# Kernel tuning notes

Hardware: AMD Instinct MI355X
Metric: run time of the kernel (lower is better)

## Reference

```python
import jax, jax.numpy as jnp
import numpy as np

B, S, D = 2, 2048, 1024
NUM_HEAD = 8
HEAD_SIZE = D // NUM_HEAD


def setup_inputs() -> dict:
    key = jax.random.key(0)
    ks = jax.random.split(key, 10)
    scale = 1.0 / np.sqrt(D)
    inp = {
        "q": jax.random.normal(ks[0], (B, S, D), dtype=jnp.float32),
        "k": jax.random.normal(ks[1], (B, S, D), dtype=jnp.float32),
        "v": jax.random.normal(ks[2], (B, S, D), dtype=jnp.float32),
        "mask": jax.random.bernoulli(ks[3], 0.1, (B, 1, S, S)),
        "Wq": jax.random.normal(ks[4], (D, D), dtype=jnp.float32) * scale,
        "bq": jnp.zeros((D,), dtype=jnp.float32),
        "Wk": jax.random.normal(ks[5], (D, D), dtype=jnp.float32) * scale,
        "bk": jnp.zeros((D,), dtype=jnp.float32),
        "Wv": jax.random.normal(ks[6], (D, D), dtype=jnp.float32) * scale,
        "bv": jnp.zeros((D,), dtype=jnp.float32),
    }
    return inp


def _split_heads(x):
    # [B,S,D] -> [B,H,S,Hd]
    b, s, _ = x.shape
    return x.reshape(b, s, NUM_HEAD, HEAD_SIZE).transpose(0, 2, 1, 3)


def reference(q, k, v, mask, Wq, bq, Wk, bk, Wv, bv):
    Q = _split_heads(q @ Wq + bq)
    K = _split_heads(k @ Wk + bk)
    V = _split_heads(v @ Wv + bv)
    # scores [B,H,S,S]; NB: mask applied BEFORE scaling, as in the original
    QK = jnp.einsum("bhqd,bhkd->bhqk", Q, K)
    QK = jnp.where(mask, jnp.float32(-1e6), QK)
    QK = QK / jnp.float32(np.sqrt(HEAD_SIZE))
    attn = jax.nn.softmax(QK, axis=-1)  # dropout is identity in eval mode
    ctx = jnp.einsum("bhqk,bhkd->bhqd", attn, V)
    out = ctx.transpose(0, 2, 1, 3).reshape(q.shape[0], q.shape[1], D)
    return out
```

## Files before the change

### kernel.cpp

```cpp
#include <hip/hip_runtime.h>

typedef __bf16 bf16;
typedef __attribute__((ext_vector_type(8))) __bf16 bf16x8;
typedef __attribute__((ext_vector_type(4))) __bf16 bf16x4;
typedef __attribute__((ext_vector_type(4))) float f32x4;
typedef __attribute__((ext_vector_type(4))) float fvec4;

#define NB 2
#define SEQ 2048
#define DM 1024
#define NH 8
#define HD 128

#define QSCL (0.08838834764831845f * 1.4426950408889634f)

#define AS1 __attribute__((address_space(1)))
#define AS3 __attribute__((address_space(3)))

__global__ __launch_bounds__(256) void prep_kernel(
    const float* __restrict__ qi, const float* __restrict__ ki,
    const float* __restrict__ vi,
    const float* __restrict__ Wq, const float* __restrict__ Wk,
    const float* __restrict__ Wv,
    const unsigned int* __restrict__ mask32,
    bf16* __restrict__ Xc, bf16* __restrict__ Wt,
    unsigned int* __restrict__ flag)
{
    const int z   = blockIdx.y;
    const int tid = threadIdx.x;
    __shared__ __align__(16) bf16 tile[64][80];
    __shared__ unsigned int sred[256];

    if (z < 3) {
        const float* src = (z == 0) ? qi : (z == 1) ? ki : vi;
        bf16* dst = Xc + (size_t)z * ((size_t)NB * SEQ * DM);
        const size_t base = (size_t)blockIdx.x * 4096 + (size_t)tid * 16;
        fvec4 f[4];
        #pragma unroll
        for (int j = 0; j < 4; j++)
            f[j] = *(const fvec4*)(src + base + j * 4);
        bf16x8 h0, h1;
        #pragma unroll
        for (int e = 0; e < 8; e++) {
            h0[e] = (bf16)f[e >> 2][e & 3];
            h1[e] = (bf16)f[2 + (e >> 2)][e & 3];
        }
        *(bf16x8*)(dst + base)     = h0;
        *(bf16x8*)(dst + base + 8) = h1;
    } else if (z < 6) {
        if (blockIdx.x >= 256) return;
        const float* W = (z == 3) ? Wq : (z == 4) ? Wk : Wv;
        bf16* dst = Wt + (size_t)(z - 3) * ((size_t)DM * DM);
        const float scl = (z == 3) ? QSCL : 1.0f;
        const int n0 = (blockIdx.x & 15) * 64;
        const int k0 = (blockIdx.x >> 4) * 64;
        #pragma unroll
        for (int p = 0; p < 4; p++) {
            const int r = p * 16 + (tid >> 4);
            const int c = (tid & 15) * 4;
            const fvec4 wv = *(const fvec4*)(W + (size_t)(k0 + r) * DM + n0 + c);
            #pragma unroll
            for (int j = 0; j < 4; j++)
                tile[c + j][r] = (bf16)(wv[j] * scl);
        }
        __syncthreads();
        #pragma unroll
        for (int p = 0; p < 2; p++) {
            const int row = p * 32 + (tid >> 3);
            const int ch  = tid & 7;
            const bf16x8 hv = *(const bf16x8*)(&tile[row][ch * 8]);
            *(bf16x8*)(dst + (size_t)(n0 + row) * DM + k0 + ch * 8) = hv;
        }
    } else {
        if (blockIdx.x != 0) return;
        unsigned int f = 0;
        for (int i = tid; i < 1024; i += 256) {
            const unsigned int w2 = mask32[i];
            if ((w2 & 0xFEFEFEFEu) == 0u && (w2 & 0xFFFFFF00u) != 0u) f = 1;
        }
        sred[tid] = f;
        __syncthreads();
        if (tid == 0) {
            unsigned int r = 0;
            for (int i = 0; i < 256; i++) r |= sred[i];
            *flag = r;
        }
    }
}

__global__ __launch_bounds__(256) void proj_kernel(
    const bf16* __restrict__ Xc, const bf16* __restrict__ Wt,
    const float* __restrict__ bq, const float* __restrict__ bk,
    const float* __restrict__ bv,
    bf16* __restrict__ Qo, bf16* __restrict__ Ko, bf16* __restrict__ Vto,
    const void* __restrict__ mask, const unsigned int* __restrict__ flag,
    unsigned long long* __restrict__ bits)
{
    __shared__ __align__(16) bf16 As[2][128 * 64];
    __shared__ __align__(16) bf16 Bs[2][128 * 64];

    const int pz = blockIdx.z;
    const int tid = threadIdx.x;

    if (pz == 3) {
        const bool bytem = (*flag & 1u) != 0;
        const int wid = blockIdx.y * 8 + blockIdx.x;
        const int t   = wid * 256 + tid;
        unsigned short* const bits16o = (unsigned short*)bits;
        #pragma unroll 2
        for (int it = 0; it < 8; ++it) {
            const size_t e0 = ((size_t)it * 65536 + t) * 16;
            unsigned int b16 = 0;
            if (bytem) {
                const uint4 wv = *(const uint4*)((const unsigned char*)mask + e0);
                const unsigned int wd[4] = {wv.x, wv.y, wv.z, wv.w};
                #pragma unroll
                for (int j = 0; j < 4; j++) {
                    b16 |= ((wd[j] & 0x000000FFu) ? 1u : 0u) << (4 * j + 0);
                    b16 |= ((wd[j] & 0x0000FF00u) ? 1u : 0u) << (4 * j + 1);
                    b16 |= ((wd[j] & 0x00FF0000u) ? 1u : 0u) << (4 * j + 2);
                    b16 |= ((wd[j] & 0xFF000000u) ? 1u : 0u) << (4 * j + 3);
                }
            } else {
                const unsigned int* mw = (const unsigned int*)mask + e0;
                #pragma unroll
                for (int j = 0; j < 4; j++) {
                    const uint4 wv = *(const uint4*)(mw + 4 * j);
                    b16 |= (wv.x ? 1u : 0u) << (4 * j + 0);
                    b16 |= (wv.y ? 1u : 0u) << (4 * j + 1);
                    b16 |= (wv.z ? 1u : 0u) << (4 * j + 2);
                    b16 |= (wv.w ? 1u : 0u) << (4 * j + 3);
                }
            }
            bits16o[e0 >> 4] = (unsigned short)b16;
        }
        return;
    }

    const bf16* X  = Xc + (size_t)pz * ((size_t)NB * SEQ * DM);
    const bf16* Bt = Wt + (size_t)pz * ((size_t)DM * DM);
    const float* bias = (pz == 0) ? bq : (pz == 1) ? bk : bv;
    const float bscl  = (pz == 0) ? QSCL : 1.0f;
    bf16* dst = (pz == 0) ? Qo : (pz == 1) ? Ko : Vto;

    const int lane = tid & 63;
    const int w    = tid >> 6;
    const int q16  = lane >> 4;
    const int l15  = lane & 15;

    const int lid  = (int)blockIdx.x + 8 * (int)blockIdx.y;
    const int nlid = (lid & 7) * 32 + (lid >> 3);
    const int m0 = (nlid >> 3) * 128;
    const int n0 = (nlid & 7) * 128;
    const int wm = (w >> 1) * 64;
    const int wn = (w & 1) * 64;

    auto stage = [&](int buf, int k0) {
        #pragma unroll
        for (int i = 0; i < 4; i++) {
            const int c   = i * 256 + tid;
            const int row = c >> 3;
            const int cir = c & 7;
            const bf16* src =
                X + (size_t)(m0 + row) * DM + k0 + ((cir ^ (row & 7)) << 3);
            __builtin_amdgcn_global_load_lds(
                (const AS1 void*)src,
                (AS3 void*)(&As[buf][c * 8]),
                16, 0, 0);
        }
        #pragma unroll
        for (int i = 0; i < 4; i++) {
            const int c   = i * 256 + tid;
            const int row = c >> 3;
            const int cir = c & 7;
            const bf16* src =
                Bt + (size_t)(n0 + row) * DM + k0 + ((cir ^ (row & 7)) << 3);
            __builtin_amdgcn_global_load_lds(
                (const AS1 void*)src,
                (AS3 void*)(&Bs[buf][c * 8]),
                16, 0, 0);
        }
    };

    f32x4 acc[4][4] = {};
    stage(0, 0);
    __syncthreads();
    int cur = 0;

    for (int kt = 0; kt < DM / 64; ++kt) {
        if (kt + 1 < DM / 64) stage(cur ^ 1, (kt + 1) * 64);
        const bf16* Asb = &As[cur][0];
        const bf16* Bsb = &Bs[cur][0];
        #pragma unroll
        for (int c2 = 0; c2 < 2; c2++) {
            bf16x8 af[4], bfr[4];
            #pragma unroll
            for (int mi = 0; mi < 4; mi++) {
                const int row = wm + mi * 16 + l15;
                af[mi] = *(const bf16x8*)(
                    Asb + row * 64 + (((c2 * 4 + q16) ^ (row & 7)) << 3));
            }
            #pragma unroll
            for (int ni = 0; ni < 4; ni++) {
                const int row = wn + ni * 16 + l15;
                bfr[ni] = *(const bf16x8*)(
                    Bsb + row * 64 + (((c2 * 4 + q16) ^ (row & 7)) << 3));
            }
            #pragma unroll
            for (int mi = 0; mi < 4; mi++)
                #pragma unroll
                for (int ni = 0; ni < 4; ni++)
                    acc[mi][ni] = __builtin_amdgcn_mfma_f32_16x16x32_bf16(
                        af[mi], bfr[ni], acc[mi][ni], 0, 0, 0);
        }
        __syncthreads();
        cur ^= 1;
    }

    float bias_v[4];
    #pragma unroll
    for (int ni = 0; ni < 4; ni++)
        bias_v[ni] = bias[n0 + wn + ni * 16 + l15];

    #pragma unroll
    for (int mi = 0; mi < 4; mi++) {
        #pragma unroll
        for (int ni = 0; ni < 4; ni++) {
            const int n  = n0 + wn + ni * 16 + l15;
            const int h  = n >> 7;
            const int hd = n & (HD - 1);
            #pragma unroll
            for (int r = 0; r < 4; r++) {
                const int m = m0 + wm + mi * 16 + q16 * 4 + r;
                const int b = m >> 11;
                const int s = m & (SEQ - 1);
                const float val = acc[mi][ni][r] + bias_v[ni] * bscl;
                size_t idx;
                if (pz == 2) {
                    const int s63 = s & 63;
                    const int nf  = s63 >> 4;
                    const int g   = (s63 >> 2) & 3;
                    const int rr  = s63 & 3;
                    const int slot = (nf >> 1) * 32 + g * 8 + (nf & 1) * 4 + rr;
                    const int sp = (s & ~63) | slot;
                    idx = ((size_t)(b * NH + h) * HD + hd) * SEQ + sp;
                } else {
                    idx = ((size_t)(b * NH + h) * SEQ + s) * HD + hd;
                }
                dst[idx] = (bf16)val;
            }
        }
    }
}

__global__ __launch_bounds__(256) void attn_kernel(
    const bf16* __restrict__ Q, const bf16* __restrict__ K,
    const bf16* __restrict__ Vt, const unsigned int* __restrict__ maskbits,
    float* __restrict__ out)
{
    __shared__ __align__(16) bf16 Ks[2][64 * 128];
    __shared__ __align__(16) bf16 Vs[2][128 * 64];

    const int tid  = threadIdx.x;
    const int lane = tid & 63;
    const int w    = tid >> 6;
    const int q16  = lane >> 4;
    const int l15  = lane & 15;
    const int l3   = l15 & 7;

    const int lid  = (int)blockIdx.x
                   + 32 * ((int)blockIdx.y + 8 * (int)blockIdx.z);
    const int nlid = (lid & 7) * 64 + (lid >> 3);
    const int q0  = (nlid & 31) * 64;
    const int bh  = nlid >> 5;
    const int b   = bh >> 3;
    const int h   = bh & 7;

    const bf16* Qb = Q  + (size_t)bh * SEQ * HD;
    const bf16* Kb = K  + (size_t)bh * SEQ * HD;
    const bf16* Vb = Vt + (size_t)bh * HD * SEQ;

    const int q_l = q0 + w * 16 + l15;
    const unsigned long long* mrowL =
        (const unsigned long long*)maskbits + (size_t)b * (SEQ * SEQ / 64)
        + (size_t)q_l * (SEQ / 64);

    bf16x8 qf[4];
    #pragma unroll
    for (int c = 0; c < 4; c++)
        qf[c] = *(const bf16x8*)(Qb + (size_t)q_l * HD + c * 32 + q16 * 8);

    f32x4 o[8] = {};
    float m_l = -__builtin_inff();
    float l_l = 0.f;

    const float MASKV = -1.0e6f * QSCL;

    auto stage = [&](int buf, int k0) {
        bf16* kd = &Ks[buf][0];
        bf16* vd = &Vs[buf][0];
        #pragma unroll
        for (int i = 0; i < 4; i++) {
            const int c   = i * 256 + tid;
            const int row = c >> 4;
            const int cir = c & 15;
            const bf16* src =
                Kb + (size_t)(k0 + row) * HD + ((cir ^ (row & 7)) << 3);
            __builtin_amdgcn_global_load_lds(
                (const AS1 void*)src,
                (AS3 void*)(kd + c * 8),
                16, 0, 0);
        }
        #pragma unroll
        for (int i = 0; i < 4; i++) {
            const int c   = i * 256 + tid;
            const int d   = c >> 3;
            const int cir = c & 7;
            const bf16* src =
                Vb + (size_t)d * SEQ + k0 + ((cir ^ (d & 7)) << 3);
            __builtin_amdgcn_global_load_lds(
                (const AS1 void*)src,
                (AS3 void*)(vd + c * 8),
                16, 0, 0);
        }
    };

    stage(0, 0);
    unsigned long long mwn = mrowL[0];
    __syncthreads();

    int cur = 0;

    for (int kt = 0; kt < SEQ / 64; ++kt) {
        const unsigned long long mwv = mwn;

        if (kt + 1 < SEQ / 64) stage(cur ^ 1, (kt + 1) * 64);
        mwn = mrowL[(kt + 1) & (SEQ / 64 - 1)];

        const bf16* Ksb = &Ks[cur][0];
        const bf16* Vsb = &Vs[cur][0];

        f32x4 sf[4] = {};
        __builtin_amdgcn_s_setprio(1);
        #pragma unroll
        for (int c = 0; c < 4; c++) {
            #pragma unroll
            for (int nf = 0; nf < 4; nf++) {
                const bf16x8 kf = *(const bf16x8*)(
                    Ksb + (nf * 16 + l15) * 128 + (((c * 4 + q16) ^ l3) << 3));
                sf[nf] = __builtin_amdgcn_mfma_f32_16x16x32_bf16(
                    kf, qf[c], sf[nf], 0, 0, 0);
            }
        }
        __builtin_amdgcn_s_setprio(0);

        #pragma unroll
        for (int nf = 0; nf < 4; nf++)
            #pragma unroll
            for (int r = 0; r < 4; r++) {
                const int mk = (int)((mwv >> (nf * 16 + q16 * 4 + r)) & 1ull);
                sf[nf][r] = mk ? MASKV : sf[nf][r];
            }

        float t0 = fmaxf(fmaxf(sf[0][0], sf[0][1]), fmaxf(sf[0][2], sf[0][3]));
        float t1 = fmaxf(fmaxf(sf[1][0], sf[1][1]), fmaxf(sf[1][2], sf[1][3]));
        float t2 = fmaxf(fmaxf(sf[2][0], sf[2][1]), fmaxf(sf[2][2], sf[2][3]));
        float t3 = fmaxf(fmaxf(sf[3][0], sf[3][1]), fmaxf(sf[3][2], sf[3][3]));
        float mx = fmaxf(fmaxf(t0, t1), fmaxf(t2, t3));
        mx = fmaxf(mx, __shfl_xor(mx, 16));
        mx = fmaxf(mx, __shfl_xor(mx, 32));
        const float mnew  = fmaxf(m_l, mx);
        const float alpha = __builtin_amdgcn_exp2f(m_l - mnew);
        const bool  need  = mnew > m_l;
        m_l = mnew;

        float ps = 0.f;
        #pragma unroll
        for (int nf = 0; nf < 4; nf++)
            #pragma unroll
            for (int r = 0; r < 4; r++) {
                const float p = __builtin_amdgcn_exp2f(sf[nf][r] - mnew);
                sf[nf][r] = p;
                ps += p;
            }
        l_l = l_l * alpha + ps;

        if (__ballot(need)) {
            #pragma unroll
            for (int df = 0; df < 8; df++)
                #pragma unroll
                for (int r = 0; r < 4; r++)
                    o[df][r] *= alpha;
        }

        bf16x8 pf[2];
        #pragma unroll
        for (int cc = 0; cc < 2; cc++) {
            bf16x8 t;
            #pragma unroll
            for (int j = 0; j < 8; j++)
                t[j] = (bf16)sf[2 * cc + (j >> 2)][j & 3];
            pf[cc] = t;
        }

        __builtin_amdgcn_s_setprio(1);
        #pragma unroll
        for (int df = 0; df < 8; df++) {
            #pragma unroll
            for (int cc = 0; cc < 2; cc++) {
                const bf16x8 vf = *(const bf16x8*)(
                    Vsb + (df * 16 + l15) * 64 + (((cc * 4 + q16) ^ l3) << 3));
                o[df] = __builtin_amdgcn_mfma_f32_16x16x32_bf16(
                    vf, pf[cc], o[df], 0, 0, 0);
            }
        }
        __builtin_amdgcn_s_setprio(0);

        __syncthreads();
        cur ^= 1;
    }

    float ls = l_l;
    ls += __shfl_xor(ls, 16);
    ls += __shfl_xor(ls, 32);
    const float linv = 1.0f / ls;

    #pragma unroll
    for (int df = 0; df < 8; df++) {
        #pragma unroll
        for (int r = 0; r < 4; r++) {
            out[((size_t)b * SEQ + q_l) * DM + h * HD + df * 16 + q16 * 4 + r] =
                o[df][r] * linv;
        }
    }
}

extern "C" void kernel_launch(void* const* d_in, const int* in_sizes, int n_in,
                              void* d_out, int out_size, void* d_ws, size_t ws_size,
                              hipStream_t stream) {
    const float* q    = (const float*)d_in[0];
    const float* k    = (const float*)d_in[1];
    const float* v    = (const float*)d_in[2];
    const void*  mask = d_in[3];
    const float* Wq   = (const float*)d_in[4];
    const float* bq   = (const float*)d_in[5];
    const float* Wk   = (const float*)d_in[6];
    const float* bk   = (const float*)d_in[7];
    const float* Wv   = (const float*)d_in[8];
    const float* bv   = (const float*)d_in[9];
    float* out = (float*)d_out;

    char* ws = (char*)d_ws;
    unsigned long long* bits = (unsigned long long*)ws;
    const size_t bits_bytes = (size_t)NB * SEQ * SEQ / 8;
    unsigned int* flag = (unsigned int*)(ws + bits_bytes);
    bf16* Qp = (bf16*)(ws + bits_bytes + 256);
    bf16* Kp = Qp + (size_t)NB * SEQ * DM;
    bf16* Vp = Kp + (size_t)NB * SEQ * DM;
    bf16* Xc = Vp + (size_t)NB * SEQ * DM;
    bf16* Wt = Xc + (size_t)3 * NB * SEQ * DM;

    prep_kernel<<<dim3(1024, 7), 256, 0, stream>>>(
        q, k, v, Wq, Wk, Wv, (const unsigned int*)mask, Xc, Wt, flag);

    dim3 pgrid(DM / 128, (NB * SEQ) / 128, 4);
    proj_kernel<<<pgrid, 256, 0, stream>>>(Xc, Wt, bq, bk, bv, Qp, Kp, Vp,
                                           mask, flag, bits);

    dim3 agrid(SEQ / 64, NH, NB);
    attn_kernel<<<agrid, 256, 0, stream>>>(Qp, Kp, Vp,
                                           (const unsigned int*)bits, out);
}
```

Measured before the change: 248.5 us.

## Software-pipeline QK^T one tile ahead with triple-buffered K in LDS

Restructures the attention loop so the QK^T MFMAs for tile t+1 are issued before the softmax and PV of tile t, letting the MFMA work overlap the exp/max VALU work. K gets a third LDS buffer, staged two tiles ahead, and V stays double-buffered. This raises LDS use and register pressure because a second score accumulator set is held, which could lower occupancy. The compiler may also serialize the code anyway.

```diff
diff --git a/kernel.cpp b/kernel.cpp
--- a/kernel.cpp
+++ b/kernel.cpp
@@ -258,7 +258,7 @@
     const bf16* __restrict__ Vt, const unsigned int* __restrict__ maskbits,
     float* __restrict__ out)
 {
-    __shared__ __align__(16) bf16 Ks[2][64 * 128];
+    __shared__ __align__(16) bf16 Ks[3][64 * 128];
     __shared__ __align__(16) bf16 Vs[2][128 * 64];
 
     const int tid  = threadIdx.x;
@@ -296,9 +296,8 @@
 
     const float MASKV = -1.0e6f * QSCL;
 
-    auto stage = [&](int buf, int k0) {
+    auto stageK = [&](int buf, int k0) {
         bf16* kd = &Ks[buf][0];
-        bf16* vd = &Vs[buf][0];
         #pragma unroll
         for (int i = 0; i < 4; i++) {
             const int c   = i * 256 + tid;
@@ -311,6 +310,9 @@
                 (AS3 void*)(kd + c * 8),
                 16, 0, 0);
         }
+    };
+    auto stageV = [&](int buf, int k0) {
+        bf16* vd = &Vs[buf][0];
         #pragma unroll
         for (int i = 0; i < 4; i++) {
             const int c   = i * 256 + tid;
@@ -325,22 +327,9 @@
         }
     };
 
-    stage(0, 0);
-    unsigned long long mwn = mrowL[0];
-    __syncthreads();
-
-    int cur = 0;
-
-    for (int kt = 0; kt < SEQ / 64; ++kt) {
-        const unsigned long long mwv = mwn;
-
-        if (kt + 1 < SEQ / 64) stage(cur ^ 1, (kt + 1) * 64);
-        mwn = mrowL[(kt + 1) & (SEQ / 64 - 1)];
-
-        const bf16* Ksb = &Ks[cur][0];
-        const bf16* Vsb = &Vs[cur][0];
-
-        f32x4 sf[4] = {};
+    auto qk = [&](const bf16* Ksb, f32x4 sf[4]) {
+        #pragma unroll
+        for (int nf = 0; nf < 4; nf++) sf[nf] = f32x4{0.f, 0.f, 0.f, 0.f};
         __builtin_amdgcn_s_setprio(1);
         #pragma unroll
         for (int c = 0; c < 4; c++) {
@@ -353,19 +342,44 @@
             }
         }
         __builtin_amdgcn_s_setprio(0);
+    };
+
+    stageK(0, 0);
+    stageK(1, 64);
+    stageV(0, 0);
+    unsigned long long mwn = mrowL[0];
+    __syncthreads();
+
+    f32x4 sfA[4], sfB[4];
+    qk(&Ks[0][0], sfA);
+
+    int cur = 0;
+    int kn = 1, kstage = 2, kfree = 0;
+
+    for (int t = 0; t < SEQ / 64; ++t) {
+        const unsigned long long mwv = mwn;
+        mwn = mrowL[(t + 1) & (SEQ / 64 - 1)];
+
+        if (t + 2 < SEQ / 64) stageK(kstage, (t + 2) * 64);
+        if (t + 1 < SEQ / 64) {
+            stageV(cur ^ 1, (t + 1) * 64);
+            qk(&Ks[kn][0], sfB);
+        }
+
+        const bf16* Vsb = &Vs[cur][0];
 
         #pragma unroll
         for (int nf = 0; nf < 4; nf++)
             #pragma unroll
             for (int r = 0; r < 4; r++) {
                 const int mk = (int)((mwv >> (nf * 16 + q16 * 4 + r)) & 1ull);
-                sf[nf][r] = mk ? MASKV : sf[nf][r];
-            }
-
-        float t0 = fmaxf(fmaxf(sf[0][0], sf[0][1]), fmaxf(sf[0][2], sf[0][3]));
-        float t1 = fmaxf(fmaxf(sf[1][0], sf[1][1]), fmaxf(sf[1][2], sf[1][3]));
-        float t2 = fmaxf(fmaxf(sf[2][0], sf[2][1]), fmaxf(sf[2][2], sf[2][3]));
-        float t3 = fmaxf(fmaxf(sf[3][0], sf[3][1]), fmaxf(sf[3][2], sf[3][3]));
+                sfA[nf][r] = mk ? MASKV : sfA[nf][r];
+            }
+
+        float t0 = fmaxf(fmaxf(sfA[0][0], sfA[0][1]), fmaxf(sfA[0][2], sfA[0][3]));
+        float t1 = fmaxf(fmaxf(sfA[1][0], sfA[1][1]), fmaxf(sfA[1][2], sfA[1][3]));
+        float t2 = fmaxf(fmaxf(sfA[2][0], sfA[2][1]), fmaxf(sfA[2][2], sfA[2][3]));
+        float t3 = fmaxf(fmaxf(sfA[3][0], sfA[3][1]), fmaxf(sfA[3][2], sfA[3][3]));
         float mx = fmaxf(fmaxf(t0, t1), fmaxf(t2, t3));
         mx = fmaxf(mx, __shfl_xor(mx, 16));
         mx = fmaxf(mx, __shfl_xor(mx, 32));
@@ -379,8 +393,8 @@
         for (int nf = 0; nf < 4; nf++)
             #pragma unroll
             for (int r = 0; r < 4; r++) {
-                const float p = __builtin_amdgcn_exp2f(sf[nf][r] - mnew);
-                sf[nf][r] = p;
+                const float p = __builtin_amdgcn_exp2f(sfA[nf][r] - mnew);
+                sfA[nf][r] = p;
                 ps += p;
             }
         l_l = l_l * alpha + ps;
@@ -396,11 +410,11 @@
         bf16x8 pf[2];
         #pragma unroll
         for (int cc = 0; cc < 2; cc++) {
-            bf16x8 t;
+            bf16x8 tt;
             #pragma unroll
             for (int j = 0; j < 8; j++)
-                t[j] = (bf16)sf[2 * cc + (j >> 2)][j & 3];
-            pf[cc] = t;
+                tt[j] = (bf16)sfA[2 * cc + (j >> 2)][j & 3];
+            pf[cc] = tt;
         }
 
         __builtin_amdgcn_s_setprio(1);
@@ -417,6 +431,11 @@
         __builtin_amdgcn_s_setprio(0);
 
         __syncthreads();
+
+        #pragma unroll
+        for (int nf = 0; nf < 4; nf++) sfA[nf] = sfB[nf];
+        const int kf_ = kfree;
+        kfree = kn; kn = kstage; kstage = kf_;
         cur ^= 1;
     }
 
```

New measurement: 250.3 us. No clear change (+0.7%).
